# Kernel optimization log

Hardware: AMD Instinct MI355X
Metric: run time of the kernel (lower is better)

The kernel has to match this reference:

```python
import jax, jax.numpy as jnp
import numpy as np

N_MIN = 5
N_MAX = 16
VARIANTS_PER_N = 16
NUM_HIDDEN = 2
HIDDEN = 512
TOTAL_MODELS = (N_MAX - N_MIN + 1) * VARIANTS_PER_N  # 192
BATCH = 65536


def setup_inputs() -> dict:
    key = jax.random.key(0)
    ks = jax.random.split(key, 8)
    n = 16
    s_in = 1.0 / np.sqrt(n)
    s_h = 1.0 / np.sqrt(HIDDEN)
    return {
        "T": jax.random.normal(ks[0], (BATCH, n), dtype=jnp.float32),
        "n": n,
        "variant_index": 3,
        "w_in": jax.random.normal(ks[1], (TOTAL_MODELS, HIDDEN, N_MAX), dtype=jnp.float32) * s_in,
        "b_in": jax.random.normal(ks[2], (TOTAL_MODELS, HIDDEN), dtype=jnp.float32) * 0.01,
        "w_hid": jax.random.normal(ks[3], (TOTAL_MODELS, NUM_HIDDEN, HIDDEN, HIDDEN), dtype=jnp.float32) * s_h,
        "b_hid": jax.random.normal(ks[4], (TOTAL_MODELS, NUM_HIDDEN, HIDDEN), dtype=jnp.float32) * 0.01,
        "w_out": jax.random.normal(ks[5], (TOTAL_MODELS, N_MAX + 1, HIDDEN), dtype=jnp.float32) * s_h,
        "b_out": jax.random.normal(ks[6], (TOTAL_MODELS, N_MAX + 1), dtype=jnp.float32) * 0.01,
    }


def _distortion(X, n):
    # X: (B, n+1). Z[:, n-1-i] = sum_j X[:, j] * X[:, j+i+1] (zero-padded shift).
    # lag k = i+1 -> column n-k; loop is over fixed small n (<=16), unrolls statically.
    cols = [jnp.sum(X[:, :-k] * X[:, k:], axis=1) for k in range(1, n + 1)]
    return jnp.stack(cols[::-1], axis=1)  # (B, n)


def reference(T, n, variant_index, w_in, b_in, w_hid, b_hid, w_out, b_out):
    model_idx = (n - N_MIN) * VARIANTS_PER_N + variant_index
    wi = w_in[model_idx]    # (H, N_MAX)
    bi = b_in[model_idx]    # (H,)
    wh = w_hid[model_idx]   # (2, H, H)
    bh = b_hid[model_idx]   # (2, H)
    wo = w_out[model_idx]   # (N_MAX+1, H)
    bo = b_out[model_idx]   # (N_MAX+1,)

    T_pad = jnp.pad(T, ((0, 0), (0, N_MAX - n)))  # (B, N_MAX)
    norm = jnp.sqrt(jnp.clip(jnp.sum(T_pad * T_pad, axis=1, keepdims=True), 1e-12))
    T_unit = T_pad / norm
    scale = jnp.sqrt(norm)

    x = jax.nn.silu(T_unit @ wi.T + bi)
    for h in range(NUM_HIDDEN):
        x = jax.nn.relu(x @ wh[h].T + bh[h])
    x_full = (x @ wo.T + bo) * scale  # (B, N_MAX+1)

    X_hat = x_full[:, :n + 1]
    X_hat_clamped = jnp.clip(X_hat, -2.0, 2.0)
    error = jnp.mean((_distortion(X_hat, n) - T) ** 2)
    error_clamped = jnp.mean((_distortion(X_hat_clamped, n) - T) ** 2)
    return (X_hat, error, X_hat_clamped, error_clamped)
```

## Files before the change

kernel.cpp:

```cpp
#include <hip/hip_runtime.h>

#define BATCH 65536
#define MT 64

typedef unsigned short u16;
typedef __bf16 bf16x8 __attribute__((ext_vector_type(8)));
typedef float f32x4 __attribute__((ext_vector_type(4)));

#define WI_OFF 0
#define WH_OFF 16384
#define WO_OFF 540672
#define WS_USH 557056
#define BI_F 0
#define BH_F 512
#define BO_F 1536
#define PART_F 1568
#define PREP_WH 65536
#define PREP_WI 2048
#define PREP_WO 2048
#define PREP_SC 1568
#define PREP_TOTAL (PREP_WH + PREP_WI + PREP_WO + PREP_SC)

__device__ inline u16 f2bf(float f) {
  union { float f; unsigned u; } v; v.f = f;
  unsigned u = v.u + 0x7fffu + ((v.u >> 16) & 1u);
  return (u16)(u >> 16);
}

__global__ void prep_kernel(const float* __restrict__ w_in, const float* __restrict__ b_in,
                            const float* __restrict__ w_hid, const float* __restrict__ b_hid,
                            const float* __restrict__ w_out, const float* __restrict__ b_out,
                            const int* __restrict__ variant, int n,
                            u16* __restrict__ wsu, float* __restrict__ wsf)
{
  const int model = (n - 5) * 16 + variant[0];
  const int i = blockIdx.x * 256 + threadIdx.x;
  if (i < PREP_WH) {
    int g = i & 3, col = (i >> 2) & 511, K32 = (i >> 11) & 15, l = i >> 15;
    const float* src = w_hid + (size_t)model * 524288 + (size_t)l * 262144 + col * 512 + K32 * 32 + g * 8;
    u16* dst = wsu + WH_OFF + (size_t)i * 8;
    #pragma unroll
    for (int e = 0; e < 8; ++e) dst[e] = f2bf(src[e]);
  } else if (i < PREP_WH + PREP_WI) {
    int j = i - PREP_WH;
    int g = j & 3, col = j >> 2;
    u16* dst = wsu + WI_OFF + (size_t)j * 8;
    #pragma unroll
    for (int e = 0; e < 8; ++e) {
      int k = g * 8 + e;
      dst[e] = (k < 16) ? f2bf(w_in[(size_t)model * 8192 + col * 16 + k]) : (u16)0;
    }
  } else if (i < PREP_WH + PREP_WI + PREP_WO) {
    int j = i - PREP_WH - PREP_WI;
    int g = j & 3, col = (j >> 2) & 31, K32 = j >> 7;
    u16* dst = wsu + WO_OFF + (size_t)j * 8;
    #pragma unroll
    for (int e = 0; e < 8; ++e) {
      int k = K32 * 32 + g * 8 + e;
      dst[e] = (col < 17) ? f2bf(w_out[(size_t)model * 8704 + col * 512 + k]) : (u16)0;
    }
  } else if (i < PREP_TOTAL) {
    int j = i - PREP_WH - PREP_WI - PREP_WO;
    if (j < 512)       wsf[BI_F + j] = b_in[(size_t)model * 512 + j];
    else if (j < 1536) wsf[BH_F + (j - 512)] = b_hid[(size_t)model * 1024 + (j - 512)];
    else               { int o = j - 1536; wsf[BO_F + o] = (o < 17) ? b_out[(size_t)model * 17 + o] : 0.f; }
  }
}

__device__ __forceinline__ bf16x8 rdA(const char* xb, int row, int kbyte) {
  return *reinterpret_cast<const bf16x8*>(xb + row * 1024 + (kbyte ^ ((row & 15) << 4)));
}
__device__ __forceinline__ void st16(char* xb, int row, int col, u16 v) {
  *(u16*)(xb + row * 1024 + ((col * 2) ^ ((row & 15) << 4))) = v;
}

template<int NK>
__device__ __forceinline__ void dense_layer(const u16* __restrict__ Wp,
                                            const float* __restrict__ bias, int act,
                                            char* xb, int l15, int q, int c0, int koff)
{
  f32x4 acc[4][4];
  #pragma unroll
  for (int a = 0; a < 4; ++a)
    #pragma unroll
    for (int b = 0; b < 4; ++b) { f32x4 z = {0.f, 0.f, 0.f, 0.f}; acc[a][b] = z; }

  const u16* Wl = Wp + (c0 + l15) * 32 + q * 8;

  if constexpr (NK == 1) {
    uint4 b0[4];
    #pragma unroll
    for (int ct = 0; ct < 4; ++ct)
      b0[ct] = *reinterpret_cast<const uint4*>(Wl + ct * 512);
    const int kb = q * 16;
    #pragma unroll
    for (int mt = 0; mt < 4; ++mt) {
      bf16x8 a = rdA(xb, mt * 16 + l15, kb);
      #pragma unroll
      for (int ct = 0; ct < 4; ++ct)
        acc[mt][ct] = __builtin_amdgcn_mfma_f32_16x16x32_bf16(
            a, __builtin_bit_cast(bf16x8, b0[ct]), acc[mt][ct], 0, 0, 0);
    }
  } else {
    uint4 bc[4], bn[4];
    {
      const u16* p = Wl + (size_t)koff * 16384;
      #pragma unroll
      for (int ct = 0; ct < 4; ++ct)
        bc[ct] = *reinterpret_cast<const uint4*>(p + ct * 512);
    }
    #pragma unroll 1
    for (int i = 0; i < NK; i += 2) {
      {
        const int Kb = (i + 1) ^ koff;
        const u16* p = Wl + (size_t)Kb * 16384;
        #pragma unroll
        for (int ct = 0; ct < 4; ++ct)
          bn[ct] = *reinterpret_cast<const uint4*>(p + ct * 512);
      }
      {
        const int kb = ((i ^ koff) * 64) + q * 16;
        #pragma unroll
        for (int mt = 0; mt < 4; ++mt) {
          bf16x8 a = rdA(xb, mt * 16 + l15, kb);
          #pragma unroll
          for (int ct = 0; ct < 4; ++ct)
            acc[mt][ct] = __builtin_amdgcn_mfma_f32_16x16x32_bf16(
                a, __builtin_bit_cast(bf16x8, bc[ct]), acc[mt][ct], 0, 0, 0);
        }
      }
      {
        const int Kc = ((i + 2) & (NK - 1)) ^ koff;
        const u16* p = Wl + (size_t)Kc * 16384;
        #pragma unroll
        for (int ct = 0; ct < 4; ++ct)
          bc[ct] = *reinterpret_cast<const uint4*>(p + ct * 512);
      }
      {
        const int kb = (((i + 1) ^ koff) * 64) + q * 16;
        #pragma unroll
        for (int mt = 0; mt < 4; ++mt) {
          bf16x8 a = rdA(xb, mt * 16 + l15, kb);
          #pragma unroll
          for (int ct = 0; ct < 4; ++ct)
            acc[mt][ct] = __builtin_amdgcn_mfma_f32_16x16x32_bf16(
                a, __builtin_bit_cast(bf16x8, bn[ct]), acc[mt][ct], 0, 0, 0);
        }
      }
    }
  }
  __syncthreads();

  float bv[4];
  #pragma unroll
  for (int ct = 0; ct < 4; ++ct) bv[ct] = bias[c0 + ct * 16 + l15];
  #pragma unroll
  for (int mt = 0; mt < 4; ++mt)
    #pragma unroll
    for (int ct = 0; ct < 4; ++ct)
      #pragma unroll
      for (int j = 0; j < 4; ++j) {
        int row = mt * 16 + q * 4 + j;
        float z = acc[mt][ct][j] + bv[ct];
        float h = act ? fmaxf(z, 0.f) : z / (1.f + __expf(-z));
        st16(xb, row, c0 + ct * 16 + l15, f2bf(h));
      }
  __syncthreads();
}

template<int CN>
__global__ __launch_bounds__(512, 4) void fused_kernel(
    const float* __restrict__ T, const u16* __restrict__ wsu,
    const float* __restrict__ wsf, float* __restrict__ Xout, float* __restrict__ Xcout,
    float* __restrict__ errPart, int n_arg)
{
  const int n = CN ? CN : n_arg;
  __shared__ u16 xs[MT * 512];
  __shared__ float xo[MT * 20];
  __shared__ float scaleS[MT];
  __shared__ float ered[8][2];

  const int tid = threadIdx.x;
  const int blk = blockIdx.x;
  const int lane = tid & 63;
  const int wid = tid >> 6;
  const int l15 = lane & 15;
  const int q = lane >> 4;
  const int c0 = wid * 64;
  const int koff = (blk >> 3) & 15;
  char* xb = (char*)xs;

  {
    const int r = tid >> 3, j = tid & 7;
    const size_t gr = (size_t)blk * MT + r;
    const float* tp = T + gr * n;
    const int k0 = 2 * j, k1 = 2 * j + 1;
    float v0 = (k0 < n) ? tp[k0] : 0.f;
    float v1 = (k1 < n) ? tp[k1] : 0.f;
    float ss = v0 * v0 + v1 * v1;
    ss += __shfl_xor(ss, 1); ss += __shfl_xor(ss, 2); ss += __shfl_xor(ss, 4);
    float norm = sqrtf(ss < 1e-12f ? 1e-12f : ss);
    float rn = 1.f / norm;
    if (j == 0) scaleS[r] = sqrtf(norm);
    st16(xb, r, k0, f2bf(v0 * rn));
    st16(xb, r, k1, f2bf(v1 * rn));
    st16(xb, r, 16 + k0, 0);
    st16(xb, r, 16 + k1, 0);
  }
  __syncthreads();

  dense_layer<1 >(wsu + WI_OFF,          wsf + BI_F,       0, xb, l15, q, c0, 0);
  dense_layer<16>(wsu + WH_OFF,          wsf + BH_F,       1, xb, l15, q, c0, koff);
  dense_layer<16>(wsu + WH_OFF + 262144, wsf + BH_F + 512, 1, xb, l15, q, c0, koff);

  if (wid < 4) {
    f32x4 oacc[2];
    { f32x4 z = {0.f, 0.f, 0.f, 0.f}; oacc[0] = z; oacc[1] = z; }
    const int bofs2 = l15 * 32 + q * 8;
    uint4 ob[2], on[2];
    #pragma unroll
    for (int ct = 0; ct < 2; ++ct)
      ob[ct] = *reinterpret_cast<const uint4*>(wsu + WO_OFF + bofs2 + ct * 512);
    #pragma unroll
    for (int K2 = 0; K2 < 16; K2 += 2) {
      #pragma unroll
      for (int ct = 0; ct < 2; ++ct)
        on[ct] = *reinterpret_cast<const uint4*>(wsu + WO_OFF + (K2 + 1) * 1024 + bofs2 + ct * 512);
      {
        bf16x8 a = rdA(xb, wid * 16 + l15, K2 * 64 + q * 16);
        #pragma unroll
        for (int ct = 0; ct < 2; ++ct)
          oacc[ct] = __builtin_amdgcn_mfma_f32_16x16x32_bf16(
              a, __builtin_bit_cast(bf16x8, ob[ct]), oacc[ct], 0, 0, 0);
      }
      if (K2 + 2 < 16) {
        #pragma unroll
        for (int ct = 0; ct < 2; ++ct)
          ob[ct] = *reinterpret_cast<const uint4*>(wsu + WO_OFF + (K2 + 2) * 1024 + bofs2 + ct * 512);
      }
      {
        bf16x8 a = rdA(xb, wid * 16 + l15, (K2 + 1) * 64 + q * 16);
        #pragma unroll
        for (int ct = 0; ct < 2; ++ct)
          oacc[ct] = __builtin_amdgcn_mfma_f32_16x16x32_bf16(
              a, __builtin_bit_cast(bf16x8, on[ct]), oacc[ct], 0, 0, 0);
      }
    }
    #pragma unroll
    for (int ct = 0; ct < 2; ++ct)
      #pragma unroll
      for (int j = 0; j < 4; ++j) {
        int o = ct * 16 + l15;
        int row = wid * 16 + q * 4 + j;
        if (o <= n) {
          float val = (oacc[ct][j] + wsf[BO_F + o]) * scaleS[row];
          size_t gr = (size_t)blk * MT + row;
          float cv = fminf(fmaxf(val, -2.f), 2.f);
          Xout[gr * (n + 1) + o] = val;
          Xcout[gr * (n + 1) + o] = cv;
          xo[row * 20 + o] = val;
        }
      }
  }
  __syncthreads();

  {
    const int r = tid >> 3, j = tid & 7;
    const size_t gr = (size_t)blk * MT + r;
    float x[17], cx[17];
    #pragma unroll
    for (int i = 0; i < 17; ++i) {
      float v = (i <= n) ? xo[r * 20 + i] : 0.f;
      x[i] = v; cx[i] = fminf(fmaxf(v, -2.f), 2.f);
    }
    float e = 0.f, ec = 0.f;
    #pragma unroll
    for (int kk = 0; kk < 2; ++kk) {
      int k = j + 1 + kk * 8;
      if (k <= n) {
        float d = 0.f, dc = 0.f;
        #pragma unroll
        for (int i = 0; i < 16; ++i) {
          if (i + k <= 16) {
            if (i + k <= n) { d += x[i] * x[i + k]; dc += cx[i] * cx[i + k]; }
          }
        }
        float tvv = T[gr * n + (n - k)];
        float r1 = d - tvv, r2 = dc - tvv;
        e += r1 * r1; ec += r2 * r2;
      }
    }
    e += __shfl_xor(e, 1);  ec += __shfl_xor(ec, 1);
    e += __shfl_xor(e, 2);  ec += __shfl_xor(ec, 2);
    e += __shfl_xor(e, 4);  ec += __shfl_xor(ec, 4);
    e += __shfl_xor(e, 8);  ec += __shfl_xor(ec, 8);
    e += __shfl_xor(e, 16); ec += __shfl_xor(ec, 16);
    e += __shfl_xor(e, 32); ec += __shfl_xor(ec, 32);
    if (lane == 0) { ered[wid][0] = e; ered[wid][1] = ec; }
  }
  __syncthreads();
  if (tid == 0) {
    float e = 0.f, ec = 0.f;
    #pragma unroll
    for (int w = 0; w < 8; ++w) { e += ered[w][0]; ec += ered[w][1]; }
    errPart[blk * 2]     = e;
    errPart[blk * 2 + 1] = ec;
  }
}

__global__ void finalize_kernel(const float* __restrict__ part, float* __restrict__ e0,
                                float* __restrict__ e1, float inv)
{
  __shared__ float se[4][2];
  const int t = threadIdx.x;
  float e = 0.f, ec = 0.f;
  for (int b = t; b < BATCH / MT; b += 256) { e += part[2 * b]; ec += part[2 * b + 1]; }
  e += __shfl_xor(e, 1);  ec += __shfl_xor(ec, 1);
  e += __shfl_xor(e, 2);  ec += __shfl_xor(ec, 2);
  e += __shfl_xor(e, 4);  ec += __shfl_xor(ec, 4);
  e += __shfl_xor(e, 8);  ec += __shfl_xor(ec, 8);
  e += __shfl_xor(e, 16); ec += __shfl_xor(ec, 16);
  e += __shfl_xor(e, 32); ec += __shfl_xor(ec, 32);
  if ((t & 63) == 0) { se[t >> 6][0] = e; se[t >> 6][1] = ec; }
  __syncthreads();
  if (t == 0) {
    float te = 0.f, tec = 0.f;
    #pragma unroll
    for (int w = 0; w < 4; ++w) { te += se[w][0]; tec += se[w][1]; }
    e0[0] = te * inv;
    e1[0] = tec * inv;
  }
}

extern "C" void kernel_launch(void* const* d_in, const int* in_sizes, int n_in,
                              void* d_out, int out_size, void* d_ws, size_t ws_size,
                              hipStream_t stream)
{
  const float* T       = (const float*)d_in[0];
  const int*   variant = (const int*)d_in[2];
  const float* w_in    = (const float*)d_in[3];
  const float* b_in    = (const float*)d_in[4];
  const float* w_hid   = (const float*)d_in[5];
  const float* b_hid   = (const float*)d_in[6];
  const float* w_out   = (const float*)d_in[7];
  const float* b_out   = (const float*)d_in[8];
  const int n = in_sizes[0] / BATCH;

  u16* wsu = (u16*)d_ws;
  float* wsf = (float*)((char*)d_ws + (size_t)WS_USH * 2);
  float* out = (float*)d_out;
  const size_t xe = (size_t)BATCH * (n + 1);
  float* Xo  = out;
  float* eP  = out + xe;
  float* Xc  = out + xe + 1;
  float* ecP = out + 2 * xe + 1;

  const int prepBlocks = (PREP_TOTAL + 255) / 256;
  prep_kernel<<<prepBlocks, 256, 0, stream>>>(w_in, b_in, w_hid, b_hid, w_out, b_out,
                                              variant, n, wsu, wsf);
  if (n == 16)
    fused_kernel<16><<<BATCH / MT, 512, 0, stream>>>(T, wsu, wsf, Xo, Xc, wsf + PART_F, n);
  else
    fused_kernel<0><<<BATCH / MT, 512, 0, stream>>>(T, wsu, wsf, Xo, Xc, wsf + PART_F, n);
  finalize_kernel<<<1, 256, 0, stream>>>(wsf + PART_F, eP, ecP, 1.f / (float)((size_t)BATCH * n));
}
```

Before: 145.6 us.

## Double the per-block row tile to reuse weight fragments across more rows

Raises the rows per block from 64 to 128. Each wave now keeps two sets of 4x4 MFMA accumulators, so every loaded weight fragment is applied to twice as many rows, which halves global/L2 weight traffic per row. The output layer now runs on all 8 waves, and the prologue and epilogue thread mappings are reshaped to 4 threads per row. In exchange, LDS use doubles, accumulator register pressure doubles, launch bounds drop to 2 blocks per CU, and the grid is halved, which lowers occupancy and the latency hiding it provides.

```diff
diff --git a/kernel.cpp b/kernel.cpp
--- a/kernel.cpp
+++ b/kernel.cpp
@@ -1,7 +1,8 @@
 #include <hip/hip_runtime.h>
 
 #define BATCH 65536
-#define MT 64
+#define MT 128
+#define NBLK (BATCH / MT)
 
 typedef unsigned short u16;
 typedef __bf16 bf16x8 __attribute__((ext_vector_type(8)));
@@ -79,11 +80,13 @@
                                             const float* __restrict__ bias, int act,
                                             char* xb, int l15, int q, int c0, int koff)
 {
-  f32x4 acc[4][4];
+  f32x4 acc[2][4][4];
   #pragma unroll
-  for (int a = 0; a < 4; ++a)
-    #pragma unroll
-    for (int b = 0; b < 4; ++b) { f32x4 z = {0.f, 0.f, 0.f, 0.f}; acc[a][b] = z; }
+  for (int p = 0; p < 2; ++p)
+    #pragma unroll
+    for (int a = 0; a < 4; ++a)
+      #pragma unroll
+      for (int b = 0; b < 4; ++b) { f32x4 z = {0.f, 0.f, 0.f, 0.f}; acc[p][a][b] = z; }
 
   const u16* Wl = Wp + (c0 + l15) * 32 + q * 8;
 
@@ -94,13 +97,15 @@
       b0[ct] = *reinterpret_cast<const uint4*>(Wl + ct * 512);
     const int kb = q * 16;
     #pragma unroll
-    for (int mt = 0; mt < 4; ++mt) {
-      bf16x8 a = rdA(xb, mt * 16 + l15, kb);
-      #pragma unroll
-      for (int ct = 0; ct < 4; ++ct)
-        acc[mt][ct] = __builtin_amdgcn_mfma_f32_16x16x32_bf16(
-            a, __builtin_bit_cast(bf16x8, b0[ct]), acc[mt][ct], 0, 0, 0);
-    }
+    for (int p = 0; p < 2; ++p)
+      #pragma unroll
+      for (int mt = 0; mt < 4; ++mt) {
+        bf16x8 a = rdA(xb, p * 64 + mt * 16 + l15, kb);
+        #pragma unroll
+        for (int ct = 0; ct < 4; ++ct)
+          acc[p][mt][ct] = __builtin_amdgcn_mfma_f32_16x16x32_bf16(
+              a, __builtin_bit_cast(bf16x8, b0[ct]), acc[p][mt][ct], 0, 0, 0);
+      }
   } else {
     uint4 bc[4], bn[4];
     {
@@ -121,13 +126,15 @@
       {
         const int kb = ((i ^ koff) * 64) + q * 16;
         #pragma unroll
-        for (int mt = 0; mt < 4; ++mt) {
-          bf16x8 a = rdA(xb, mt * 16 + l15, kb);
+        for (int p = 0; p < 2; ++p)
           #pragma unroll
-          for (int ct = 0; ct < 4; ++ct)
-            acc[mt][ct] = __builtin_amdgcn_mfma_f32_16x16x32_bf16(
-                a, __builtin_bit_cast(bf16x8, bc[ct]), acc[mt][ct], 0, 0, 0);
-        }
+          for (int mt = 0; mt < 4; ++mt) {
+            bf16x8 a = rdA(xb, p * 64 + mt * 16 + l15, kb);
+            #pragma unroll
+            for (int ct = 0; ct < 4; ++ct)
+              acc[p][mt][ct] = __builtin_amdgcn_mfma_f32_16x16x32_bf16(
+                  a, __builtin_bit_cast(bf16x8, bc[ct]), acc[p][mt][ct], 0, 0, 0);
+          }
       }
       {
         const int Kc = ((i + 2) & (NK - 1)) ^ koff;
@@ -139,13 +146,15 @@
       {
         const int kb = (((i + 1) ^ koff) * 64) + q * 16;
         #pragma unroll
-        for (int mt = 0; mt < 4; ++mt) {
-          bf16x8 a = rdA(xb, mt * 16 + l15, kb);
+        for (int p = 0; p < 2; ++p)
           #pragma unroll
-          for (int ct = 0; ct < 4; ++ct)
-            acc[mt][ct] = __builtin_amdgcn_mfma_f32_16x16x32_bf16(
-                a, __builtin_bit_cast(bf16x8, bn[ct]), acc[mt][ct], 0, 0, 0);
-        }
+          for (int mt = 0; mt < 4; ++mt) {
+            bf16x8 a = rdA(xb, p * 64 + mt * 16 + l15, kb);
+            #pragma unroll
+            for (int ct = 0; ct < 4; ++ct)
+              acc[p][mt][ct] = __builtin_amdgcn_mfma_f32_16x16x32_bf16(
+                  a, __builtin_bit_cast(bf16x8, bn[ct]), acc[p][mt][ct], 0, 0, 0);
+          }
       }
     }
   }
@@ -155,21 +164,23 @@
   #pragma unroll
   for (int ct = 0; ct < 4; ++ct) bv[ct] = bias[c0 + ct * 16 + l15];
   #pragma unroll
-  for (int mt = 0; mt < 4; ++mt)
-    #pragma unroll
-    for (int ct = 0; ct < 4; ++ct)
-      #pragma unroll
-      for (int j = 0; j < 4; ++j) {
-        int row = mt * 16 + q * 4 + j;
-        float z = acc[mt][ct][j] + bv[ct];
-        float h = act ? fmaxf(z, 0.f) : z / (1.f + __expf(-z));
-        st16(xb, row, c0 + ct * 16 + l15, f2bf(h));
-      }
+  for (int p = 0; p < 2; ++p)
+    #pragma unroll
+    for (int mt = 0; mt < 4; ++mt)
+      #pragma unroll
+      for (int ct = 0; ct < 4; ++ct)
+        #pragma unroll
+        for (int j = 0; j < 4; ++j) {
+          int row = p * 64 + mt * 16 + q * 4 + j;
+          float z = acc[p][mt][ct][j] + bv[ct];
+          float h = act ? fmaxf(z, 0.f) : z / (1.f + __expf(-z));
+          st16(xb, row, c0 + ct * 16 + l15, f2bf(h));
+        }
   __syncthreads();
 }
 
 template<int CN>
-__global__ __launch_bounds__(512, 4) void fused_kernel(
+__global__ __launch_bounds__(512, 2) void fused_kernel(
     const float* __restrict__ T, const u16* __restrict__ wsu,
     const float* __restrict__ wsf, float* __restrict__ Xout, float* __restrict__ Xcout,
     float* __restrict__ errPart, int n_arg)
@@ -191,21 +202,25 @@
   char* xb = (char*)xs;
 
   {
-    const int r = tid >> 3, j = tid & 7;
+    const int r = tid >> 2, j = tid & 3;
     const size_t gr = (size_t)blk * MT + r;
     const float* tp = T + gr * n;
-    const int k0 = 2 * j, k1 = 2 * j + 1;
-    float v0 = (k0 < n) ? tp[k0] : 0.f;
-    float v1 = (k1 < n) ? tp[k1] : 0.f;
-    float ss = v0 * v0 + v1 * v1;
-    ss += __shfl_xor(ss, 1); ss += __shfl_xor(ss, 2); ss += __shfl_xor(ss, 4);
+    float v[4]; float ss = 0.f;
+    #pragma unroll
+    for (int c = 0; c < 4; ++c) {
+      int k = j * 4 + c;
+      v[c] = (k < n) ? tp[k] : 0.f;
+      ss += v[c] * v[c];
+    }
+    ss += __shfl_xor(ss, 1); ss += __shfl_xor(ss, 2);
     float norm = sqrtf(ss < 1e-12f ? 1e-12f : ss);
     float rn = 1.f / norm;
     if (j == 0) scaleS[r] = sqrtf(norm);
-    st16(xb, r, k0, f2bf(v0 * rn));
-    st16(xb, r, k1, f2bf(v1 * rn));
-    st16(xb, r, 16 + k0, 0);
-    st16(xb, r, 16 + k1, 0);
+    #pragma unroll
+    for (int c = 0; c < 4; ++c) {
+      st16(xb, r, j * 4 + c, f2bf(v[c] * rn));
+      st16(xb, r, 16 + j * 4 + c, 0);
+    }
   }
   __syncthreads();
 
@@ -213,7 +228,7 @@
   dense_layer<16>(wsu + WH_OFF,          wsf + BH_F,       1, xb, l15, q, c0, koff);
   dense_layer<16>(wsu + WH_OFF + 262144, wsf + BH_F + 512, 1, xb, l15, q, c0, koff);
 
-  if (wid < 4) {
+  {
     f32x4 oacc[2];
     { f32x4 z = {0.f, 0.f, 0.f, 0.f}; oacc[0] = z; oacc[1] = z; }
     const int bofs2 = l15 * 32 + q * 8;
@@ -265,7 +280,7 @@
   __syncthreads();
 
   {
-    const int r = tid >> 3, j = tid & 7;
+    const int r = tid >> 2, j = tid & 3;
     const size_t gr = (size_t)blk * MT + r;
     float x[17], cx[17];
     #pragma unroll
@@ -275,8 +290,8 @@
     }
     float e = 0.f, ec = 0.f;
     #pragma unroll
-    for (int kk = 0; kk < 2; ++kk) {
-      int k = j + 1 + kk * 8;
+    for (int kk = 0; kk < 4; ++kk) {
+      int k = j + 1 + kk * 4;
       if (k <= n) {
         float d = 0.f, dc = 0.f;
         #pragma unroll
@@ -314,7 +329,7 @@
   __shared__ float se[4][2];
   const int t = threadIdx.x;
   float e = 0.f, ec = 0.f;
-  for (int b = t; b < BATCH / MT; b += 256) { e += part[2 * b]; ec += part[2 * b + 1]; }
+  for (int b = t; b < NBLK; b += 256) { e += part[2 * b]; ec += part[2 * b + 1]; }
   e += __shfl_xor(e, 1);  ec += __shfl_xor(ec, 1);
   e += __shfl_xor(e, 2);  ec += __shfl_xor(ec, 2);
   e += __shfl_xor(e, 4);  ec += __shfl_xor(ec, 4);
@@ -359,8 +374,8 @@
   prep_kernel<<<prepBlocks, 256, 0, stream>>>(w_in, b_in, w_hid, b_hid, w_out, b_out,
                                               variant, n, wsu, wsf);
   if (n == 16)
-    fused_kernel<16><<<BATCH / MT, 512, 0, stream>>>(T, wsu, wsf, Xo, Xc, wsf + PART_F, n);
+    fused_kernel<16><<<NBLK, 512, 0, stream>>>(T, wsu, wsf, Xo, Xc, wsf + PART_F, n);
   else
-    fused_kernel<0><<<BATCH / MT, 512, 0, stream>>>(T, wsu, wsf, Xo, Xc, wsf + PART_F, n);
+    fused_kernel<0><<<NBLK, 512, 0, stream>>>(T, wsu, wsf, Xo, Xc, wsf + PART_F, n);
   finalize_kernel<<<1, 256, 0, stream>>>(wsf + PART_F, eP, ecP, 1.f / (float)((size_t)BATCH * n));
 }
```

Result: faster. 135.6 us (-6.8%).

## Double row tile to 128 with 1024-thread blocks and narrower per-wave column slices

Applied to the files above, without the earlier changes.

Raises the per-block row tile from 64 to 128 and the block size to 16 waves, so each weight fragment loaded from global memory feeds 8 row tiles instead of 4 and weight traffic per row is halved. Each wave now owns 32 output columns. The output layer is spread across all waves, the per-block K-offset rotation is removed, and T is cached in LDS for the error pass. In exchange it roughly doubles LDS per block, yields half as many blocks, and drops the staggered K start that spread weight reads across blocks.

```diff
diff --git a/kernel.cpp b/kernel.cpp
--- a/kernel.cpp
+++ b/kernel.cpp
@@ -1,7 +1,8 @@
 #include <hip/hip_runtime.h>
 
 #define BATCH 65536
-#define MT 64
+#define MT 128
+#define NBLK (BATCH / MT)
 
 typedef unsigned short u16;
 typedef __bf16 bf16x8 __attribute__((ext_vector_type(8)));
@@ -77,72 +78,67 @@
 template<int NK>
 __device__ __forceinline__ void dense_layer(const u16* __restrict__ Wp,
                                             const float* __restrict__ bias, int act,
-                                            char* xb, int l15, int q, int c0, int koff)
-{
-  f32x4 acc[4][4];
+                                            char* xb, int l15, int q, int c0)
+{
+  f32x4 acc[8][2];
   #pragma unroll
-  for (int a = 0; a < 4; ++a)
-    #pragma unroll
-    for (int b = 0; b < 4; ++b) { f32x4 z = {0.f, 0.f, 0.f, 0.f}; acc[a][b] = z; }
+  for (int a = 0; a < 8; ++a)
+    #pragma unroll
+    for (int b = 0; b < 2; ++b) { f32x4 z = {0.f, 0.f, 0.f, 0.f}; acc[a][b] = z; }
 
   const u16* Wl = Wp + (c0 + l15) * 32 + q * 8;
 
   if constexpr (NK == 1) {
-    uint4 b0[4];
-    #pragma unroll
-    for (int ct = 0; ct < 4; ++ct)
+    uint4 b0[2];
+    #pragma unroll
+    for (int ct = 0; ct < 2; ++ct)
       b0[ct] = *reinterpret_cast<const uint4*>(Wl + ct * 512);
     const int kb = q * 16;
     #pragma unroll
-    for (int mt = 0; mt < 4; ++mt) {
+    for (int mt = 0; mt < 8; ++mt) {
       bf16x8 a = rdA(xb, mt * 16 + l15, kb);
       #pragma unroll
-      for (int ct = 0; ct < 4; ++ct)
+      for (int ct = 0; ct < 2; ++ct)
         acc[mt][ct] = __builtin_amdgcn_mfma_f32_16x16x32_bf16(
             a, __builtin_bit_cast(bf16x8, b0[ct]), acc[mt][ct], 0, 0, 0);
     }
   } else {
-    uint4 bc[4], bn[4];
-    {
-      const u16* p = Wl + (size_t)koff * 16384;
-      #pragma unroll
-      for (int ct = 0; ct < 4; ++ct)
-        bc[ct] = *reinterpret_cast<const uint4*>(p + ct * 512);
-    }
+    uint4 bc[2], bn[2];
+    #pragma unroll
+    for (int ct = 0; ct < 2; ++ct)
+      bc[ct] = *reinterpret_cast<const uint4*>(Wl + ct * 512);
     #pragma unroll 1
     for (int i = 0; i < NK; i += 2) {
       {
-        const int Kb = (i + 1) ^ koff;
-        const u16* p = Wl + (size_t)Kb * 16384;
-        #pragma unroll
-        for (int ct = 0; ct < 4; ++ct)
+        const u16* p = Wl + (size_t)(i + 1) * 16384;
+        #pragma unroll
+        for (int ct = 0; ct < 2; ++ct)
           bn[ct] = *reinterpret_cast<const uint4*>(p + ct * 512);
       }
       {
-        const int kb = ((i ^ koff) * 64) + q * 16;
-        #pragma unroll
-        for (int mt = 0; mt < 4; ++mt) {
+        const int kb = i * 64 + q * 16;
+        #pragma unroll
+        for (int mt = 0; mt < 8; ++mt) {
           bf16x8 a = rdA(xb, mt * 16 + l15, kb);
           #pragma unroll
-          for (int ct = 0; ct < 4; ++ct)
+          for (int ct = 0; ct < 2; ++ct)
             acc[mt][ct] = __builtin_amdgcn_mfma_f32_16x16x32_bf16(
                 a, __builtin_bit_cast(bf16x8, bc[ct]), acc[mt][ct], 0, 0, 0);
         }
       }
       {
-        const int Kc = ((i + 2) & (NK - 1)) ^ koff;
-        const u16* p = Wl + (size_t)Kc * 16384;
-        #pragma unroll
-        for (int ct = 0; ct < 4; ++ct)
+        const u16* p = Wl + (size_t)((i + 2) & (NK - 1)) * 16384;
+        #pragma unroll
+        for (int ct = 0; ct < 2; ++ct)
           bc[ct] = *reinterpret_cast<const uint4*>(p + ct * 512);
       }
       {
-        const int kb = (((i + 1) ^ koff) * 64) + q * 16;
-        #pragma unroll
-        for (int mt = 0; mt < 4; ++mt) {
+        const int kb = (i + 1) * 64 + q * 16;
+        #pragma unroll
+        for (int mt = 0; mt < 8; ++mt) {
           bf16x8 a = rdA(xb, mt * 16 + l15, kb);
           #pragma unroll
-          for (int ct = 0; ct < 4; ++ct)
+          for (int ct = 0; ct < 2; ++ct)
             acc[mt][ct] = __builtin_amdgcn_mfma_f32_16x16x32_bf16(
                 a, __builtin_bit_cast(bf16x8, bn[ct]), acc[mt][ct], 0, 0, 0);
         }
@@ -151,13 +147,13 @@
   }
   __syncthreads();
 
-  float bv[4];
+  float bv[2];
   #pragma unroll
-  for (int ct = 0; ct < 4; ++ct) bv[ct] = bias[c0 + ct * 16 + l15];
+  for (int ct = 0; ct < 2; ++ct) bv[ct] = bias[c0 + ct * 16 + l15];
   #pragma unroll
-  for (int mt = 0; mt < 4; ++mt)
-    #pragma unroll
-    for (int ct = 0; ct < 4; ++ct)
+  for (int mt = 0; mt < 8; ++mt)
+    #pragma unroll
+    for (int ct = 0; ct < 2; ++ct)
       #pragma unroll
       for (int j = 0; j < 4; ++j) {
         int row = mt * 16 + q * 4 + j;
@@ -169,7 +165,7 @@
 }
 
 template<int CN>
-__global__ __launch_bounds__(512, 4) void fused_kernel(
+__global__ __launch_bounds__(1024, 4) void fused_kernel(
     const float* __restrict__ T, const u16* __restrict__ wsu,
     const float* __restrict__ wsf, float* __restrict__ Xout, float* __restrict__ Xcout,
     float* __restrict__ errPart, int n_arg)
@@ -177,8 +173,9 @@
   const int n = CN ? CN : n_arg;
   __shared__ u16 xs[MT * 512];
   __shared__ float xo[MT * 20];
+  __shared__ float ts[MT * 16];
   __shared__ float scaleS[MT];
-  __shared__ float ered[8][2];
+  __shared__ float ered[16][2];
 
   const int tid = threadIdx.x;
   const int blk = blockIdx.x;
@@ -186,8 +183,7 @@
   const int wid = tid >> 6;
   const int l15 = lane & 15;
   const int q = lane >> 4;
-  const int c0 = wid * 64;
-  const int koff = (blk >> 3) & 15;
+  const int c0 = wid * 32;
   char* xb = (char*)xs;
 
   {
@@ -206,67 +202,54 @@
     st16(xb, r, k1, f2bf(v1 * rn));
     st16(xb, r, 16 + k0, 0);
     st16(xb, r, 16 + k1, 0);
-  }
-  __syncthreads();
-
-  dense_layer<1 >(wsu + WI_OFF,          wsf + BI_F,       0, xb, l15, q, c0, 0);
-  dense_layer<16>(wsu + WH_OFF,          wsf + BH_F,       1, xb, l15, q, c0, koff);
-  dense_layer<16>(wsu + WH_OFF + 262144, wsf + BH_F + 512, 1, xb, l15, q, c0, koff);
-
-  if (wid < 4) {
-    f32x4 oacc[2];
-    { f32x4 z = {0.f, 0.f, 0.f, 0.f}; oacc[0] = z; oacc[1] = z; }
-    const int bofs2 = l15 * 32 + q * 8;
-    uint4 ob[2], on[2];
-    #pragma unroll
-    for (int ct = 0; ct < 2; ++ct)
-      ob[ct] = *reinterpret_cast<const uint4*>(wsu + WO_OFF + bofs2 + ct * 512);
-    #pragma unroll
-    for (int K2 = 0; K2 < 16; K2 += 2) {
-      #pragma unroll
-      for (int ct = 0; ct < 2; ++ct)
-        on[ct] = *reinterpret_cast<const uint4*>(wsu + WO_OFF + (K2 + 1) * 1024 + bofs2 + ct * 512);
-      {
-        bf16x8 a = rdA(xb, wid * 16 + l15, K2 * 64 + q * 16);
-        #pragma unroll
-        for (int ct = 0; ct < 2; ++ct)
-          oacc[ct] = __builtin_amdgcn_mfma_f32_16x16x32_bf16(
-              a, __builtin_bit_cast(bf16x8, ob[ct]), oacc[ct], 0, 0, 0);
-      }
-      if (K2 + 2 < 16) {
-        #pragma unroll
-        for (int ct = 0; ct < 2; ++ct)
-          ob[ct] = *reinterpret_cast<const uint4*>(wsu + WO_OFF + (K2 + 2) * 1024 + bofs2 + ct * 512);
-      }
-      {
-        bf16x8 a = rdA(xb, wid * 16 + l15, (K2 + 1) * 64 + q * 16);
-        #pragma unroll
-        for (int ct = 0; ct < 2; ++ct)
-          oacc[ct] = __builtin_amdgcn_mfma_f32_16x16x32_bf16(
-              a, __builtin_bit_cast(bf16x8, on[ct]), oacc[ct], 0, 0, 0);
-      }
-    }
-    #pragma unroll
-    for (int ct = 0; ct < 2; ++ct)
-      #pragma unroll
-      for (int j = 0; j < 4; ++j) {
-        int o = ct * 16 + l15;
-        int row = wid * 16 + q * 4 + j;
-        if (o <= n) {
-          float val = (oacc[ct][j] + wsf[BO_F + o]) * scaleS[row];
-          size_t gr = (size_t)blk * MT + row;
-          float cv = fminf(fmaxf(val, -2.f), 2.f);
-          Xout[gr * (n + 1) + o] = val;
-          Xcout[gr * (n + 1) + o] = cv;
-          xo[row * 20 + o] = val;
-        }
-      }
+    ts[r * 16 + k0] = v0;
+    ts[r * 16 + k1] = v1;
+  }
+  __syncthreads();
+
+  dense_layer<1 >(wsu + WI_OFF,          wsf + BI_F,       0, xb, l15, q, c0);
+  dense_layer<16>(wsu + WH_OFF,          wsf + BH_F,       1, xb, l15, q, c0);
+  dense_layer<16>(wsu + WH_OFF + 262144, wsf + BH_F + 512, 1, xb, l15, q, c0);
+
+  {
+    const int rg = wid >> 1;
+    const int ct = wid & 1;
+    f32x4 oacc = {0.f, 0.f, 0.f, 0.f};
+    const u16* WoL = wsu + WO_OFF + (ct * 16 + l15) * 32 + q * 8;
+    uint4 ob = *reinterpret_cast<const uint4*>(WoL);
+    #pragma unroll 1
+    for (int K = 0; K < 16; K += 2) {
+      uint4 on = *reinterpret_cast<const uint4*>(WoL + (size_t)(K + 1) * 1024);
+      {
+        bf16x8 a = rdA(xb, rg * 16 + l15, K * 64 + q * 16);
+        oacc = __builtin_amdgcn_mfma_f32_16x16x32_bf16(
+            a, __builtin_bit_cast(bf16x8, ob), oacc, 0, 0, 0);
+      }
+      ob = *reinterpret_cast<const uint4*>(WoL + (size_t)((K + 2) & 15) * 1024);
+      {
+        bf16x8 a = rdA(xb, rg * 16 + l15, (K + 1) * 64 + q * 16);
+        oacc = __builtin_amdgcn_mfma_f32_16x16x32_bf16(
+            a, __builtin_bit_cast(bf16x8, on), oacc, 0, 0, 0);
+      }
+    }
+    const int o = ct * 16 + l15;
+    #pragma unroll
+    for (int j = 0; j < 4; ++j) {
+      int row = rg * 16 + q * 4 + j;
+      if (o <= n) {
+        float val = (oacc[j] + wsf[BO_F + o]) * scaleS[row];
+        size_t gr = (size_t)blk * MT + row;
+        float cv = fminf(fmaxf(val, -2.f), 2.f);
+        Xout[gr * (n + 1) + o] = val;
+        Xcout[gr * (n + 1) + o] = cv;
+        xo[row * 20 + o] = val;
+      }
+    }
   }
   __syncthreads();
 
   {
     const int r = tid >> 3, j = tid & 7;
-    const size_t gr = (size_t)blk * MT + r;
     float x[17], cx[17];
     #pragma unroll
     for (int i = 0; i < 17; ++i) {
@@ -285,7 +268,7 @@
             if (i + k <= n) { d += x[i] * x[i + k]; dc += cx[i] * cx[i + k]; }
           }
         }
-        float tvv = T[gr * n + (n - k)];
+        float tvv = ts[r * 16 + (n - k)];
         float r1 = d - tvv, r2 = dc - tvv;
         e += r1 * r1; ec += r2 * r2;
       }
@@ -302,7 +285,7 @@
   if (tid == 0) {
     float e = 0.f, ec = 0.f;
     #pragma unroll
-    for (int w = 0; w < 8; ++w) { e += ered[w][0]; ec += ered[w][1]; }
+    for (int w = 0; w < 16; ++w) { e += ered[w][0]; ec += ered[w][1]; }
     errPart[blk * 2]     = e;
     errPart[blk * 2 + 1] = ec;
   }
@@ -314,7 +297,7 @@
   __shared__ float se[4][2];
   const int t = threadIdx.x;
   float e = 0.f, ec = 0.f;
-  for (int b = t; b < BATCH / MT; b += 256) { e += part[2 * b]; ec += part[2 * b + 1]; }
+  for (int b = t; b < NBLK; b += 256) { e += part[2 * b]; ec += part[2 * b + 1]; }
   e += __shfl_xor(e, 1);  ec += __shfl_xor(ec, 1);
   e += __shfl_xor(e, 2);  ec += __shfl_xor(ec, 2);
   e += __shfl_xor(e, 4);  ec += __shfl_xor(ec, 4);
@@ -359,8 +342,8 @@
   prep_kernel<<<prepBlocks, 256, 0, stream>>>(w_in, b_in, w_hid, b_hid, w_out, b_out,
                                               variant, n, wsu, wsf);
   if (n == 16)
-    fused_kernel<16><<<BATCH / MT, 512, 0, stream>>>(T, wsu, wsf, Xo, Xc, wsf + PART_F, n);
+    fused_kernel<16><<<NBLK, 1024, 0, stream>>>(T, wsu, wsf, Xo, Xc, wsf + PART_F, n);
   else
-    fused_kernel<0><<<BATCH / MT, 512, 0, stream>>>(T, wsu, wsf, Xo, Xc, wsf + PART_F, n);
+    fused_kernel<0><<<NBLK, 1024, 0, stream>>>(T, wsu, wsf, Xo, Xc, wsf + PART_F, n);
   finalize_kernel<<<1, 256, 0, stream>>>(wsf + PART_F, eP, ecP, 1.f / (float)((size_t)BATCH * n));
 }
```

Result: slower. 165.8 us (+13.9%).
